# Performance work log

Measured on AMD Instinct MI355X. Metric: run time of the kernel, lower is better.

The kernel has to match this reference:

```python
import jax, jax.numpy as jnp
import numpy as np

P_SIZE = 5
NUM_HEAD = 8
GN_EPS = 1e-5


def _conv1x1(w, x, b=None):
    # w: (out_c, in_c), x: (n, in_c, h, w)
    y = jnp.einsum('oc,nchw->nohw', w, x)
    if b is not None:
        y = y + b[None, :, None, None]
    return y


def _leaky_relu(x, slope=0.2):
    return jnp.where(x >= 0, x, slope * x)


def _bilinear_sample_zeros(feat, vx, vy):
    # feat: (c, H, W); vx, vy: (p2, H, W) pixel coords (align_corners=True,
    # padding_mode='zeros'). Returns (c, p2, H, W).
    c, H, W = feat.shape
    x0 = jnp.floor(vx)
    y0 = jnp.floor(vy)
    x1 = x0 + 1.0
    y1 = y0 + 1.0
    wx1 = vx - x0
    wy1 = vy - y0
    wx0 = 1.0 - wx1
    wy0 = 1.0 - wy1

    def corner(xi, yi, wgt):
        valid = (xi >= 0) & (xi <= W - 1) & (yi >= 0) & (yi <= H - 1)
        xc = jnp.clip(xi, 0, W - 1).astype(jnp.int32)
        yc = jnp.clip(yi, 0, H - 1).astype(jnp.int32)
        g = feat[:, yc, xc]  # (c, p2, H, W)
        return g * (wgt * valid)[None]

    return (corner(x0, y0, wx0 * wy0) + corner(x1, y0, wx1 * wy0)
            + corner(x0, y1, wx0 * wy1) + corner(x1, y1, wx1 * wy1))


def _deform_coords(deform_field, h, w, p_size):
    # deform_field: (n, 2, h, w) -> vx, vy: (n, p2, h, w) pixel coords.
    pad = (p_size - 1) // 2
    gy, gx = jnp.meshgrid(jnp.arange(h, dtype=deform_field.dtype),
                          jnp.arange(w, dtype=deform_field.dtype), indexing='ij')
    shift = jnp.arange(p_size, dtype=deform_field.dtype) - pad
    sy, sx = jnp.meshgrid(shift, shift, indexing='ij')
    sy = sy.reshape(-1, 1, 1)
    sx = sx.reshape(-1, 1, 1)
    vx = gx[None] + sx + deform_field[:, None, 0]  # (n, p2, h, w)
    vy = gy[None] + sy + deform_field[:, None, 1]
    return vx, vy


def _transformer_forward(query, key, value, deform_field,
                         w_q, w_k, w_v, w_fc,
                         mlp_w1, mlp_b1, mlp_w2, mlp_b2, gn_w, gn_b):
    p2 = P_SIZE * P_SIZE
    q = _conv1x1(w_q, query)
    k = _conv1x1(w_k, key)
    v = _conv1x1(w_v, value)
    n, c, h, w = q.shape
    d_k = c // NUM_HEAD

    vx, vy = _deform_coords(deform_field, h, w, P_SIZE)
    sample = jax.vmap(_bilinear_sample_zeros)  # over batch
    k_s = sample(k, vx, vy)  # (n, c, p2, h, w)
    v_s = sample(v, vx, vy)

    qh = q.reshape(n, NUM_HEAD, d_k, h, w)
    kh = k_s.reshape(n, NUM_HEAD, d_k, p2, h, w)
    vh = v_s.reshape(n, NUM_HEAD, d_k, p2, h, w)

    scale = 1.0 / jnp.sqrt(jnp.asarray(d_k, q.dtype))
    scores = jnp.einsum('nedyx,nedpyx->neyxp', qh * scale, kh)
    attn = jax.nn.softmax(scores, axis=-1)
    out = jnp.einsum('neyxp,nedpyx->nedyx', attn, vh).reshape(n, c, h, w)
    out = _conv1x1(w_fc, out)

    hid = _leaky_relu(_conv1x1(mlp_w1, out, mlp_b1))
    out = out + _conv1x1(mlp_w2, hid, mlp_b2)

    # GroupNorm(1, c): normalize over (c, h, w) per sample
    mean = jnp.mean(out, axis=(1, 2, 3), keepdims=True)
    var = jnp.var(out, axis=(1, 2, 3), keepdims=True)
    out = (out - mean) * jax.lax.rsqrt(var + GN_EPS)
    out = out * gn_w[None, :, None, None] + gn_b[None, :, None, None]
    return out


def setup_inputs() -> dict:
    key = jax.random.key(0)
    ks = jax.random.split(key, 12)
    n, C, H, W = 1, 128, 128, 128
    hidden = C * 2
    s = 1.0 / np.sqrt(C)
    return {
        'query': jax.random.normal(ks[0], (n, C, H, W), jnp.float32),
        'key': jax.random.normal(ks[1], (n, C, H, W), jnp.float32),
        'value': jax.random.normal(ks[2], (n, C, H, W), jnp.float32),
        'deform_field': jax.random.normal(ks[3], (n, 2, H, W), jnp.float32) * 2.0,
        'w_q': jax.random.normal(ks[4], (C, C), jnp.float32) * s,
        'w_k': jax.random.normal(ks[5], (C, C), jnp.float32) * s,
        'w_v': jax.random.normal(ks[6], (C, C), jnp.float32) * s,
        'w_fc': jax.random.normal(ks[7], (C, C), jnp.float32) * s,
        'mlp_w1': jax.random.normal(ks[8], (hidden, C), jnp.float32) * s,
        'mlp_b1': jnp.zeros((hidden,), jnp.float32),
        'mlp_w2': jax.random.normal(ks[9], (C, hidden), jnp.float32) * (1.0 / np.sqrt(hidden)),
        'mlp_b2': jnp.zeros((C,), jnp.float32),
        'gn_w': jnp.ones((C,), jnp.float32),
        'gn_b': jnp.zeros((C,), jnp.float32),
    }


def reference(query, key, value, deform_field, w_q, w_k, w_v, w_fc,
              mlp_w1, mlp_b1, mlp_w2, mlp_b2, gn_w, gn_b):
    return _transformer_forward(query, key, value, deform_field,
                                w_q, w_k, w_v, w_fc,
                                mlp_w1, mlp_b1, mlp_w2, mlp_b2, gn_w, gn_b)
```

## Files before the change

kernel.cpp:

```cpp
#include <hip/hip_runtime.h>
#include <hip/hip_bf16.h>

#define HW 16384
#define W 128
#define C 128
#define HID 256

typedef __attribute__((ext_vector_type(8))) short short8v;
typedef __attribute__((ext_vector_type(4))) float f32x4;

__device__ __forceinline__ unsigned short f2bf(float f) {
    union { float f; unsigned u; } x; x.f = f;
    unsigned r = x.u + 0x7FFF + ((x.u >> 16) & 1);
    return (unsigned short)(r >> 16);
}
__device__ __forceinline__ float bf2f(unsigned short b) {
    union { unsigned u; float f; } x; x.u = ((unsigned)b) << 16;
    return x.f;
}

__device__ __forceinline__ void stage_load(const unsigned short* __restrict__ src,
                                           short8v* r, int t) {
    #pragma unroll
    for (int c = 0; c < 8; ++c)
        r[c] = *(const short8v*)(src + (size_t)(c * 256 + t) * 8);
}
template<int RSH>
__device__ __forceinline__ void stage_write(const short8v* r, unsigned short* lds, int t) {
    #pragma unroll
    for (int c = 0; c < 8; ++c) {
        int gi = c * 256 + t;
        int row = gi >> RSH, colg = gi & ((1 << RSH) - 1);
        *(short8v*)(lds + (size_t)(((row << RSH) + (colg ^ (row & 7))) << 3)) = r[c];
    }
}
template<int RSH>
__device__ __forceinline__ void stage32f(const float* __restrict__ src,
                                         unsigned short* lds, int t) {
    #pragma unroll
    for (int c = 0; c < 8; ++c) {
        int gi = c * 256 + t;
        int row = gi >> RSH, colg = gi & ((1 << RSH) - 1);
        float4 a = *(const float4*)(src + (size_t)gi * 8);
        float4 b = *(const float4*)(src + (size_t)gi * 8 + 4);
        short8v v;
        v[0] = (short)f2bf(a.x); v[1] = (short)f2bf(a.y);
        v[2] = (short)f2bf(a.z); v[3] = (short)f2bf(a.w);
        v[4] = (short)f2bf(b.x); v[5] = (short)f2bf(b.y);
        v[6] = (short)f2bf(b.z); v[7] = (short)f2bf(b.w);
        *(short8v*)(lds + (size_t)(((row << RSH) + (colg ^ (row & 7))) << 3)) = v;
    }
}

__global__ __launch_bounds__(256, 2)
void qkv_mfma(const float* __restrict__ q_in, const float* __restrict__ k_in,
              const float* __restrict__ v_in,
              const float* __restrict__ w_q, const float* __restrict__ w_k,
              const float* __restrict__ w_v,
              const float* __restrict__ wfc, const float* __restrict__ w1,
              const float* __restrict__ w2,
              unsigned short* __restrict__ wb,
              unsigned short* __restrict__ q_t, unsigned short* __restrict__ kv_t) {
    __shared__ unsigned short lx[3][32 * 128];
    __shared__ unsigned short wbuf[16384];
    const int t = threadIdx.x;
    const int p0 = blockIdx.x * 32;
    const int lane = t & 63, row16 = lane & 15, g = lane >> 4;
    const int w = t >> 6, nh = w & 1, mh = w >> 1;
    const int ploc = nh * 16 + row16;
    const int pix = p0 + ploc;
    const int swz = (ploc & 7) << 3;

    stage32f<4>(w_q, wbuf, t);

    if (t < 192) {
        int i = blockIdx.x * 192 + t;
        float v = (i < 16384) ? wfc[i] : (i < 49152) ? w1[i - 16384] : w2[i - 49152];
        wb[i] = f2bf(v);
    }

    const float* ins[3] = {q_in, k_in, v_in};
    #pragma unroll
    for (int m = 0; m < 3; ++m) {
        #pragma unroll
        for (int it = 0; it < 16; ++it) {
            int e = t + 256 * it;
            int p = e & 31, c = e >> 5;
            lx[m][p * 128 + (c ^ ((p & 7) << 3))] = f2bf(ins[m][c * HW + p0 + p]);
        }
    }

    const float* ws[3] = {w_q, w_k, w_v};
    #pragma unroll 1
    for (int m = 0; m < 3; ++m) {
        if (m > 0) {
            __syncthreads();
            stage32f<4>(ws[m], wbuf, t);
        }
        __syncthreads();

        f32x4 acc[4] = {};
        #pragma unroll
        for (int kk = 0; kk < 4; ++kk) {
            short8v b = *(const short8v*)&lx[m][ploc * 128 + ((kk * 32 + g * 8) ^ swz)];
            #pragma unroll
            for (int f = 0; f < 4; ++f) {
                int row = mh * 64 + f * 16 + row16;
                short8v a = *(const short8v*)&wbuf[(row << 7) + (((kk * 4 + g) ^ (row & 7)) << 3)];
                acc[f] = __builtin_amdgcn_mfma_f32_16x16x32_bf16(a, b, acc[f], 0, 0, 0);
            }
        }
        #pragma unroll
        for (int f = 0; f < 4; ++f) {
            int o = mh * 64 + f * 16 + g * 4;
            ushort4 st;
            st.x = f2bf(acc[f][0]); st.y = f2bf(acc[f][1]);
            st.z = f2bf(acc[f][2]); st.w = f2bf(acc[f][3]);
            if (m == 0)      *(ushort4*)&q_t[(size_t)pix * 128 + o] = st;
            else if (m == 1) *(ushort4*)&kv_t[(size_t)pix * 256 + o] = st;
            else             *(ushort4*)&kv_t[(size_t)pix * 256 + 128 + o] = st;
        }
    }
}

__global__ __launch_bounds__(256, 2)
void attn_kernel(const unsigned short* __restrict__ q_t, const unsigned short* __restrict__ kv_t,
                 const float* __restrict__ deform, unsigned short* __restrict__ ao_t) {
    const int t = threadIdx.x;
    const int pi = t >> 4;
    const int g = t & 15;
    const char* kvb = (const char*)kv_t;
    const int go = g * 16;

    const int jj = blockIdx.x;
    const int y = jj >> 3;
    const int x = ((jj & 7) << 4) + pi;
    const int pix = y * W + x;

    const float dx = deform[pix];
    const float dy = deform[HW + pix];
    const float fdx = floorf(dx), fdy = floorf(dy);
    const float fx = dx - fdx, fy = dy - fdy;
    const float wx0 = 1.f - fx, wx1 = fx, wy0 = 1.f - fy, wy1 = fy;
    const int x0 = x - 2 + (int)fdx;
    const int y0 = y - 2 + (int)fdy;

    int   coff[6], roff[6];
    float colv[6], rowv[6];
    #pragma unroll
    for (int j = 0; j < 6; ++j) {
        int xc = x0 + j, yc = y0 + j;
        colv[j] = ((unsigned)xc <= 127u) ? 1.f : 0.f;
        rowv[j] = ((unsigned)yc <= 127u) ? 1.f : 0.f;
        coff[j] = (min(max(xc, 0), 127) << 9) + go;
        roff[j] = min(max(yc, 0), 127) << 16;
    }

    float q[8];
    {
        short8v qv = *(const short8v*)(q_t + (size_t)pix * C + g * 8);
        #pragma unroll
        for (int e = 0; e < 8; ++e) q[e] = bf2f((unsigned short)qv[e]) * 0.25f;
    }

    float d[36];
    #pragma unroll
    for (int jy = 0; jy < 6; ++jy) {
        #pragma unroll
        for (int jx = 0; jx < 6; ++jx) {
            short8v k = *(const short8v*)(kvb + (roff[jy] + coff[jx]));
            float dd = 0.f;
            #pragma unroll
            for (int e = 0; e < 8; ++e) dd += q[e] * bf2f((unsigned short)k[e]);
            d[jy * 6 + jx] = dd * (rowv[jy] * colv[jx]);
        }
    }

    float s[25];
    #pragma unroll
    for (int iy = 0; iy < 5; ++iy) {
        #pragma unroll
        for (int ix = 0; ix < 5; ++ix) {
            float sp = wy0 * (wx0 * d[iy * 6 + ix]       + wx1 * d[iy * 6 + ix + 1])
                     + wy1 * (wx0 * d[(iy + 1) * 6 + ix] + wx1 * d[(iy + 1) * 6 + ix + 1]);
            sp += __shfl_xor(sp, 1);
            s[iy * 5 + ix] = sp;
        }
    }

    float m = s[0];
    #pragma unroll
    for (int p = 1; p < 25; ++p) m = fmaxf(m, s[p]);
    float sum = 0.f;
    #pragma unroll
    for (int p = 0; p < 25; ++p) {
        float e = __expf(s[p] - m);
        s[p] = e;
        sum += e;
    }
    const float inv = 1.f / sum;

    float b[36];
    #pragma unroll
    for (int jy = 0; jy < 6; ++jy) {
        #pragma unroll
        for (int jx = 0; jx < 6; ++jx) {
            float acc = 0.f;
            if (jy < 5  && jx < 5)  acc += wy0 * wx0 * s[jy * 5 + jx];
            if (jy < 5  && jx >= 1) acc += wy0 * wx1 * s[jy * 5 + jx - 1];
            if (jy >= 1 && jx < 5)  acc += wy1 * wx0 * s[(jy - 1) * 5 + jx];
            if (jy >= 1 && jx >= 1) acc += wy1 * wx1 * s[(jy - 1) * 5 + jx - 1];
            b[jy * 6 + jx] = acc * (rowv[jy] * colv[jx]);
        }
    }

    float oc[8] = {0.f, 0.f, 0.f, 0.f, 0.f, 0.f, 0.f, 0.f};
    #pragma unroll
    for (int jy = 0; jy < 6; ++jy) {
        #pragma unroll
        for (int jx = 0; jx < 6; ++jx) {
            short8v v = *(const short8v*)(kvb + (roff[jy] + coff[jx]) + 256);
            float bw = b[jy * 6 + jx];
            #pragma unroll
            for (int e = 0; e < 8; ++e) oc[e] += bw * bf2f((unsigned short)v[e]);
        }
    }

    short8v ob;
    #pragma unroll
    for (int e = 0; e < 8; ++e) ob[e] = (short)f2bf(oc[e] * inv);
    *(short8v*)(ao_t + (size_t)pix * C + g * 8) = ob;
}

__global__ __launch_bounds__(256, 2)
void mlp_mfma(const unsigned short* __restrict__ ao_t, const unsigned short* __restrict__ wb,
              const float* __restrict__ b1, const float* __restrict__ b2,
              float* __restrict__ out2, float2* __restrict__ partials) {
    __shared__ unsigned short wbuf[16384];
    __shared__ unsigned short l1[32 * 128];
    __shared__ unsigned short lh[32 * 256];
    __shared__ float rs[8];
    const int t = threadIdx.x;
    const int p0 = blockIdx.x * 32;
    const int lane = t & 63, row16 = lane & 15, g = lane >> 4;
    const int w = t >> 6, nh = w & 1, mh = w >> 1;
    const int ploc = nh * 16 + row16;
    const int pix = p0 + ploc;
    const int swz = (ploc & 7) << 3;
    const unsigned short* wfc_b = wb;
    const unsigned short* w1_b  = wb + 16384;
    const unsigned short* w2_b  = wb + 49152;

    short8v r[8];
    stage_load(wfc_b, r, t);
    short8v bf[4];
    #pragma unroll
    for (int kk = 0; kk < 4; ++kk)
        bf[kk] = *(const short8v*)&ao_t[(size_t)pix * 128 + kk * 32 + g * 8];
    stage_write<4>(r, wbuf, t);
    __syncthreads();

    stage_load(w1_b, r, t);
    {
        f32x4 acc[4] = {};
        #pragma unroll
        for (int kk = 0; kk < 4; ++kk) {
            #pragma unroll
            for (int f = 0; f < 4; ++f) {
                int row = mh * 64 + f * 16 + row16;
                short8v a = *(const short8v*)&wbuf[(row << 7) + (((kk * 4 + g) ^ (row & 7)) << 3)];
                acc[f] = __builtin_amdgcn_mfma_f32_16x16x32_bf16(a, bf[kk], acc[f], 0, 0, 0);
            }
        }
        #pragma unroll
        for (int f = 0; f < 4; ++f)
            #pragma unroll
            for (int e = 0; e < 4; ++e) {
                int o = mh * 64 + f * 16 + g * 4 + e;
                l1[ploc * 128 + (o ^ swz)] = f2bf(acc[f][e]);
            }
    }
    __syncthreads();
    stage_write<4>(r, wbuf, t);
    __syncthreads();

    #pragma unroll
    for (int s = 0; s < 2; ++s) {
        if (s == 0) stage_load(w1_b + 16384, r, t);
        else        stage_load(w2_b, r, t);
        f32x4 acc[4] = {};
        #pragma unroll
        for (int kk = 0; kk < 4; ++kk) {
            short8v b = *(const short8v*)&l1[ploc * 128 + ((kk * 32 + g * 8) ^ swz)];
            #pragma unroll
            for (int f = 0; f < 4; ++f) {
                int row = mh * 64 + f * 16 + row16;
                short8v a = *(const short8v*)&wbuf[(row << 7) + (((kk * 4 + g) ^ (row & 7)) << 3)];
                acc[f] = __builtin_amdgcn_mfma_f32_16x16x32_bf16(a, b, acc[f], 0, 0, 0);
            }
        }
        #pragma unroll
        for (int f = 0; f < 4; ++f) {
            int h = s * 128 + mh * 64 + f * 16 + g * 4;
            float4 bb = *(const float4*)&b1[h];
            float hv[4] = {acc[f][0] + bb.x, acc[f][1] + bb.y,
                           acc[f][2] + bb.z, acc[f][3] + bb.w};
            #pragma unroll
            for (int e = 0; e < 4; ++e) {
                float v = (hv[e] >= 0.f) ? hv[e] : 0.2f * hv[e];
                lh[ploc * 256 + ((h + e) ^ swz)] = f2bf(v);
            }
        }
        __syncthreads();
        if (s == 0) stage_write<4>(r, wbuf, t);
        else        stage_write<5>(r, wbuf, t);
        __syncthreads();
    }

    float lsum = 0.f, lsq = 0.f;
    #pragma unroll
    for (int s = 0; s < 2; ++s) {
        if (s == 0) stage_load(w2_b + 16384, r, t);
        f32x4 acc[2] = {};
        #pragma unroll
        for (int kk = 0; kk < 8; ++kk) {
            short8v b = *(const short8v*)&lh[ploc * 256 + ((kk * 32 + g * 8) ^ swz)];
            #pragma unroll
            for (int f = 0; f < 2; ++f) {
                int row = mh * 32 + f * 16 + row16;
                short8v a = *(const short8v*)&wbuf[(row << 8) + (((kk * 4 + g) ^ (row & 7)) << 3)];
                acc[f] = __builtin_amdgcn_mfma_f32_16x16x32_bf16(a, b, acc[f], 0, 0, 0);
            }
        }
        #pragma unroll
        for (int f = 0; f < 2; ++f) {
            int ob = s * 64 + mh * 32 + f * 16 + g * 4;
            float4 b2v = *(const float4*)&b2[ob];
            ushort4 res = *(const ushort4*)&l1[ploc * 128 + (ob ^ swz)];
            float bv[4] = {b2v.x, b2v.y, b2v.z, b2v.w};
            unsigned short rr[4] = {res.x, res.y, res.z, res.w};
            #pragma unroll
            for (int e = 0; e < 4; ++e) {
                float v = acc[f][e] + bf2f(rr[e]) + bv[e];
                out2[(size_t)(ob + e) * HW + pix] = v;
                lsum += v;
                lsq += v * v;
            }
        }
        if (s == 0) {
            __syncthreads();
            stage_write<5>(r, wbuf, t);
            __syncthreads();
        }
    }

    #pragma unroll
    for (int s = 1; s < 64; s <<= 1) {
        lsum += __shfl_xor(lsum, s);
        lsq  += __shfl_xor(lsq, s);
    }
    if (lane == 0) { rs[w] = lsum; rs[4 + w] = lsq; }
    __syncthreads();
    if (t == 0)
        partials[blockIdx.x] = make_float2(rs[0] + rs[1] + rs[2] + rs[3],
                                           rs[4] + rs[5] + rs[6] + rs[7]);
}

__global__ void norm_kernel(float* __restrict__ out2, const float2* __restrict__ partials,
                            const float* __restrict__ gn_w, const float* __restrict__ gn_b) {
    __shared__ float rs[8];
    __shared__ float stat[2];
    const int t = threadIdx.x;

    float2 p0 = partials[t];
    float2 p1 = partials[t + 256];
    float a = p0.x + p1.x, bb = p0.y + p1.y;
    #pragma unroll
    for (int s = 1; s < 64; s <<= 1) {
        a  += __shfl_xor(a, s);
        bb += __shfl_xor(bb, s);
    }
    if ((t & 63) == 0) { rs[t >> 6] = a; rs[4 + (t >> 6)] = bb; }
    __syncthreads();
    if (t == 0) {
        const float invN = 1.f / 2097152.f;
        float mean = (rs[0] + rs[1] + rs[2] + rs[3]) * invN;
        float var = (rs[4] + rs[5] + rs[6] + rs[7]) * invN - mean * mean;
        stat[0] = mean;
        stat[1] = rsqrtf(var + 1e-5f);
    }
    __syncthreads();

    const float mean = stat[0], rstd = stat[1];
    const int gid = blockIdx.x * 256 + t;
    int base = gid * 4;
    int o = base >> 14;
    float g = gn_w[o] * rstd;
    float b = gn_b[o];
    float4 v = *(const float4*)(out2 + base);
    float4 r;
    r.x = (v.x - mean) * g + b;
    r.y = (v.y - mean) * g + b;
    r.z = (v.z - mean) * g + b;
    r.w = (v.w - mean) * g + b;
    *(float4*)(out2 + base) = r;
}

extern "C" void kernel_launch(void* const* d_in, const int* in_sizes, int n_in,
                              void* d_out, int out_size, void* d_ws, size_t ws_size,
                              hipStream_t stream) {
    const float* query  = (const float*)d_in[0];
    const float* key    = (const float*)d_in[1];
    const float* value  = (const float*)d_in[2];
    const float* deform = (const float*)d_in[3];
    const float* w_q    = (const float*)d_in[4];
    const float* w_k    = (const float*)d_in[5];
    const float* w_v    = (const float*)d_in[6];
    const float* w_fc   = (const float*)d_in[7];
    const float* mlp_w1 = (const float*)d_in[8];
    const float* mlp_b1 = (const float*)d_in[9];
    const float* mlp_w2 = (const float*)d_in[10];
    const float* mlp_b2 = (const float*)d_in[11];
    const float* gn_w   = (const float*)d_in[12];
    const float* gn_b   = (const float*)d_in[13];

    float* out = (float*)d_out;
    char* wsb  = (char*)d_ws;

    unsigned short* q_t  = (unsigned short*)wsb;
    unsigned short* kv_t = (unsigned short*)(wsb + ((size_t)4 << 20));
    unsigned short* ao_t = (unsigned short*)(wsb + ((size_t)12 << 20));
    unsigned short* wb   = (unsigned short*)(wsb + ((size_t)16 << 20));
    float2* partials = (float2*)(wsb + ((size_t)17 << 20));

    qkv_mfma<<<512, 256, 0, stream>>>(query, key, value, w_q, w_k, w_v,
                                      w_fc, mlp_w1, mlp_w2, wb, q_t, kv_t);
    attn_kernel<<<1024, 256, 0, stream>>>(q_t, kv_t, deform, ao_t);
    mlp_mfma<<<512, 256, 0, stream>>>(ao_t, wb, mlp_b1, mlp_b2, out, partials);
    norm_kernel<<<2048, 256, 0, stream>>>(out, partials, gn_w, gn_b);
}
```

Measured before the change: 49.72 us.

## Vectorize QKV input loads, use bf16 fdot2 in attention, widen norm kernel

```diff
diff --git a/kernel.cpp b/kernel.cpp
--- a/kernel.cpp
+++ b/kernel.cpp
@@ -8,6 +8,19 @@
 
 typedef __attribute__((ext_vector_type(8))) short short8v;
 typedef __attribute__((ext_vector_type(4))) float f32x4;
+
+#if defined(__has_builtin)
+#if __has_builtin(__builtin_amdgcn_fdot2_f32_bf16)
+#define HAVE_FDOT2 1
+#endif
+#endif
+#ifndef HAVE_FDOT2
+#define HAVE_FDOT2 0
+#endif
+
+#if HAVE_FDOT2
+typedef __attribute__((ext_vector_type(2))) __bf16 bf16x2;
+#endif
 
 __device__ __forceinline__ unsigned short f2bf(float f) {
     union { float f; unsigned u; } x; x.f = f;
@@ -83,10 +96,17 @@
     #pragma unroll
     for (int m = 0; m < 3; ++m) {
         #pragma unroll
-        for (int it = 0; it < 16; ++it) {
-            int e = t + 256 * it;
-            int p = e & 31, c = e >> 5;
-            lx[m][p * 128 + (c ^ ((p & 7) << 3))] = f2bf(ins[m][c * HW + p0 + p]);
+        for (int i = 0; i < 4; ++i) {
+            int fid = t + 256 * i;
+            int c = fid >> 3;
+            int p4 = (fid & 7) << 2;
+            float4 v = *(const float4*)&ins[m][c * HW + p0 + p4];
+            #pragma unroll
+            for (int j = 0; j < 4; ++j) {
+                int p = p4 + j;
+                float vv = j == 0 ? v.x : j == 1 ? v.y : j == 2 ? v.z : v.w;
+                lx[m][p * 128 + (c ^ ((p & 7) << 3))] = f2bf(vv);
+            }
         }
     }
 
@@ -156,12 +176,22 @@
         roff[j] = min(max(yc, 0), 127) << 16;
     }
 
+#if HAVE_FDOT2
+    union QU { unsigned short u[8]; bf16x2 b[4]; } qu;
+    {
+        short8v qv = *(const short8v*)(q_t + (size_t)pix * C + g * 8);
+        #pragma unroll
+        for (int e = 0; e < 8; ++e)
+            qu.u[e] = f2bf(bf2f((unsigned short)qv[e]) * 0.25f);
+    }
+#else
     float q[8];
     {
         short8v qv = *(const short8v*)(q_t + (size_t)pix * C + g * 8);
         #pragma unroll
         for (int e = 0; e < 8; ++e) q[e] = bf2f((unsigned short)qv[e]) * 0.25f;
     }
+#endif
 
     float d[36];
     #pragma unroll
@@ -169,9 +199,19 @@
         #pragma unroll
         for (int jx = 0; jx < 6; ++jx) {
             short8v k = *(const short8v*)(kvb + (roff[jy] + coff[jx]));
+#if HAVE_FDOT2
+            union KU { short8v s; bf16x2 b[4]; } ku;
+            ku.s = k;
             float dd = 0.f;
+            dd = __builtin_amdgcn_fdot2_f32_bf16(ku.b[0], qu.b[0], dd, false);
+            dd = __builtin_amdgcn_fdot2_f32_bf16(ku.b[1], qu.b[1], dd, false);
+            dd = __builtin_amdgcn_fdot2_f32_bf16(ku.b[2], qu.b[2], dd, false);
+            dd = __builtin_amdgcn_fdot2_f32_bf16(ku.b[3], qu.b[3], dd, false);
+#else
+            float dd = 0.f;
             #pragma unroll
             for (int e = 0; e < 8; ++e) dd += q[e] * bf2f((unsigned short)k[e]);
+#endif
             d[jy * 6 + jx] = dd * (rowv[jy] * colv[jx]);
         }
     }
@@ -392,18 +432,23 @@
     __syncthreads();
 
     const float mean = stat[0], rstd = stat[1];
-    const int gid = blockIdx.x * 256 + t;
-    int base = gid * 4;
-    int o = base >> 14;
+    const size_t base = ((size_t)blockIdx.x * 256 + t) * 8;
+    int o = (int)(base >> 14);
     float g = gn_w[o] * rstd;
     float b = gn_b[o];
-    float4 v = *(const float4*)(out2 + base);
-    float4 r;
-    r.x = (v.x - mean) * g + b;
-    r.y = (v.y - mean) * g + b;
-    r.z = (v.z - mean) * g + b;
-    r.w = (v.w - mean) * g + b;
-    *(float4*)(out2 + base) = r;
+    float4 v0 = *(const float4*)(out2 + base);
+    float4 v1 = *(const float4*)(out2 + base + 4);
+    float4 r0, r1;
+    r0.x = (v0.x - mean) * g + b;
+    r0.y = (v0.y - mean) * g + b;
+    r0.z = (v0.z - mean) * g + b;
+    r0.w = (v0.w - mean) * g + b;
+    r1.x = (v1.x - mean) * g + b;
+    r1.y = (v1.y - mean) * g + b;
+    r1.z = (v1.z - mean) * g + b;
+    r1.w = (v1.w - mean) * g + b;
+    *(float4*)(out2 + base) = r0;
+    *(float4*)(out2 + base + 4) = r1;
 }
 
 extern "C" void kernel_launch(void* const* d_in, const int* in_sizes, int n_in,
@@ -437,5 +482,5 @@
                                       w_fc, mlp_w1, mlp_w2, wb, q_t, kv_t);
     attn_kernel<<<1024, 256, 0, stream>>>(q_t, kv_t, deform, ao_t);
     mlp_mfma<<<512, 256, 0, stream>>>(ao_t, wb, mlp_b1, mlp_b2, out, partials);
-    norm_kernel<<<2048, 256, 0, stream>>>(out, partials, gn_w, gn_b);
-}
+    norm_kernel<<<1024, 256, 0, stream>>>(out, partials, gn_w, gn_b);
+}
```

New measurement: 54.42 us. +9.5%, slower.
